# Performance work log

Hardware: AMD Instinct MI355X
Metric: run time of the kernel (lower is better)

Reference implementation:

```python
import jax, jax.numpy as jnp
import numpy as np
from jax import lax

TAU = 2.0
V_TH = 1.0
ALPHA = 4.0   # spikingjelly surrogate.Sigmoid default
BN_EPS = 1e-5
HEADS = 8


def lif(x):
    """Multi-step LIF neuron (tau=2, v_reset=0, hard reset, detach_reset).
    x: [T, ...] -> spikes [T, ...]. Forward is Heaviside; sigmoid surrogate
    is wired in via straight-through for the bwd variant."""
    def step(v, xt):
        v = v + (xt - v) / TAU                      # charge
        sg = jax.nn.sigmoid(ALPHA * (v - V_TH))     # surrogate
        hard = (v >= V_TH).astype(x.dtype)
        spike = sg + lax.stop_gradient(hard - sg)   # fwd: hard, bwd: sigmoid'
        v = v * (1.0 - lax.stop_gradient(spike))    # detached hard reset to 0
        return v, spike
    _, s = lax.scan(step, jnp.zeros_like(x[0]), x)
    return s


def conv1x1_bn(x, w, g, b, m, var, bias=None):
    # x: [N, C, H, W]; 1x1 conv == channel matmul, then eval-mode BN
    y = jnp.einsum('nchw,dc->ndhw', x, w)
    if bias is not None:
        y = y + bias[None, :, None, None]
    scale = g / jnp.sqrt(var + BN_EPS)
    shift = b - m * scale
    return y * scale[None, :, None, None] + shift[None, :, None, None]


def to_heads(x, T, B, C, H, W):
    # [T,B,C,H,W] -> [T,B,heads,N,hd]
    N = H * W
    hd = C // HEADS
    x = x.reshape(T, B, C, N).transpose(0, 1, 3, 2)          # [T,B,N,C]
    return x.reshape(T, B, N, HEADS, hd).transpose(0, 1, 3, 2, 4)


def _forward(x, q_w, q_bn_g, q_bn_b, q_bn_m, q_bn_v,
             k_w, k_bn_g, k_bn_b, k_bn_m, k_bn_v,
             v_w, v_bn_g, v_bn_b, v_bn_m, v_bn_v,
             out_w, out_b, out_bn_g, out_bn_b, out_bn_m, out_bn_v):
    T, B, C, H, W = x.shape
    N = H * W
    identity = x

    xs = lif(x)                                  # shortcut_lif
    x_qkv = xs.reshape(T * B, C, H, W)

    q = lif(conv1x1_bn(x_qkv, q_w, q_bn_g, q_bn_b, q_bn_m, q_bn_v).reshape(T, B, C, H, W))
    k = lif(conv1x1_bn(x_qkv, k_w, k_bn_g, k_bn_b, k_bn_m, k_bn_v).reshape(T, B, C, H, W))
    v = lif(conv1x1_bn(x_qkv, v_w, v_bn_g, v_bn_b, v_bn_m, v_bn_v).reshape(T, B, C, H, W))

    qh = to_heads(q, T, B, C, H, W)              # [T,B,h,N,hd]
    kh = to_heads(k, T, B, C, H, W)
    vh = to_heads(v, T, B, C, H, W)

    kv = jnp.sum(kh * vh, axis=-2, keepdims=True)   # [T,B,h,1,hd]
    kv = lif(kv)                                    # talking_heads_proj_lif
    y = qh * kv                                     # [T,B,h,N,hd]

    # [T,B,h,N,hd] -> transpose(3,4) -> [T,B,h,hd,N] -> [T,B,C,H,W]
    y = y.transpose(0, 1, 2, 4, 3).reshape(T, B, C, H, W)
    y = conv1x1_bn(y.reshape(T * B, C, H, W), out_w, out_bn_g, out_bn_b,
                   out_bn_m, out_bn_v, bias=out_b).reshape(T, B, C, H, W)
    return y + identity, vh


def setup_inputs() -> dict:
    key = jax.random.key(0)
    ks = jax.random.split(key, 6)
    T, B, C, H, W = 4, 32, 512, 14, 14
    inp = {
        'x': jax.random.normal(ks[0], (T, B, C, H, W), dtype=jnp.float32),
        'q_w': jax.random.normal(ks[1], (C, C), dtype=jnp.float32) * 0.05,
        'k_w': jax.random.normal(ks[2], (C, C), dtype=jnp.float32) * 0.05,
        'v_w': jax.random.normal(ks[3], (C, C), dtype=jnp.float32) * 0.05,
        'out_w': jax.random.normal(ks[4], (C, C), dtype=jnp.float32) * 0.05,
        'out_b': jnp.zeros((C,), dtype=jnp.float32),
    }
    for p in ('q', 'k', 'v', 'out'):
        inp[f'{p}_bn_g'] = jnp.ones((C,), dtype=jnp.float32)
        inp[f'{p}_bn_b'] = jnp.zeros((C,), dtype=jnp.float32)
        inp[f'{p}_bn_m'] = jnp.zeros((C,), dtype=jnp.float32)
        inp[f'{p}_bn_v'] = jnp.ones((C,), dtype=jnp.float32)
    return inp


def reference(x, q_w, q_bn_g, q_bn_b, q_bn_m, q_bn_v,
              k_w, k_bn_g, k_bn_b, k_bn_m, k_bn_v,
              v_w, v_bn_g, v_bn_b, v_bn_m, v_bn_v,
              out_w, out_b, out_bn_g, out_bn_b, out_bn_m, out_bn_v):
    return _forward(x, q_w, q_bn_g, q_bn_b, q_bn_m, q_bn_v,
                    k_w, k_bn_g, k_bn_b, k_bn_m, k_bn_v,
                    v_w, v_bn_g, v_bn_b, v_bn_m, v_bn_v,
                    out_w, out_b, out_bn_g, out_bn_b, out_bn_m, out_bn_v)
```

## Files before the change

kernel.cpp:

```cpp
#include <hip/hip_runtime.h>
#include <math.h>

#define T_   4
#define B_   32
#define C_   512
#define N_   196
#define TB_  128
#define M_   25088
#define BNP_ 6272
#define OUT1_ 12845056

typedef unsigned short ushort_t;
typedef __attribute__((ext_vector_type(8)))  __bf16 bf16x8;
typedef __attribute__((ext_vector_type(16))) float  f32x16;

__device__ __forceinline__ ushort_t f2bf(float f) {
    unsigned int u = __float_as_uint(f);
    u = u + 0x7FFFu + ((u >> 16) & 1u);
    return (ushort_t)(u >> 16);
}
__device__ __forceinline__ float bf2f(ushort_t h) {
    return __uint_as_float(((unsigned int)h) << 16);
}

#define GL2LDS(gp, lp) \
    __builtin_amdgcn_global_load_lds((const __attribute__((address_space(1))) void*)(gp), \
                                     (__attribute__((address_space(3))) void*)(lp), 16, 0, 0)

__global__ __launch_bounds__(256)
void prep_lifx_kernel(
    const float* __restrict__ qw, const float* __restrict__ kw,
    const float* __restrict__ vw, const float* __restrict__ ow,
    const float* __restrict__ qg, const float* __restrict__ qb, const float* __restrict__ qm, const float* __restrict__ qv,
    const float* __restrict__ kg, const float* __restrict__ kb, const float* __restrict__ km, const float* __restrict__ kvr,
    const float* __restrict__ vg, const float* __restrict__ vb, const float* __restrict__ vm, const float* __restrict__ vv,
    const float* __restrict__ og, const float* __restrict__ ob, const float* __restrict__ om, const float* __restrict__ ov,
    const float* __restrict__ obias,
    ushort_t* __restrict__ wsplit, ushort_t* __restrict__ osplit,
    float* __restrict__ scale_qkv, float* __restrict__ shift_qkv,
    float* __restrict__ scale_o,   float* __restrict__ shift_o,
    float* __restrict__ kvpart,
    const float* __restrict__ x, ushort_t* __restrict__ xs)
{
    __shared__ ushort_t tile[64 * 66];
    const int bid = blockIdx.x;
    const int tid = threadIdx.x;

    if (bid < 3072) {
        int i = bid * 256 + tid;
        int d = i >> 9, c = i & 511;
        const float* src = (d < 512) ? qw : (d < 1024) ? kw : vw;
        float wv = src[(d & 511) * 512 + c];
        ushort_t h = f2bf(wv);
        float r1 = wv - bf2f(h);
        ushort_t mm = f2bf(r1);
        wsplit[((size_t)d * 2 + 0) * 512 + c] = h;
        wsplit[((size_t)d * 2 + 1) * 512 + c] = mm;
        if (d < 512)
            osplit[(size_t)d * 512 + c] = f2bf(ow[d * 512 + c]);

        if (i < 3 * C_) {
            int p = i >> 9, dl = i & 511;
            const float* g = (p == 0) ? qg : (p == 1) ? kg : vg;
            const float* b = (p == 0) ? qb : (p == 1) ? kb : vb;
            const float* m = (p == 0) ? qm : (p == 1) ? km : vm;
            const float* r = (p == 0) ? qv : (p == 1) ? kvr : vv;
            float sc = g[dl] / sqrtf(r[dl] + 1e-5f);
            scale_qkv[i] = sc;
            shift_qkv[i] = b[dl] - m[dl] * sc;
        }
        if (i < C_) {
            float sc = og[i] / sqrtf(ov[i] + 1e-5f);
            scale_o[i] = sc;
            shift_o[i] = ob[i] - om[i] * sc + obias[i] * sc;
        }
        if (i < TB_ * C_) kvpart[i] = 0.f;
        return;
    }

    const int l = bid - 3072;
    const int n0 = (l & 3) * 64;
    const int c0 = ((l >> 2) & 7) * 64;
    const int b  = l >> 5;
    const int j = tid & 63, w = tid >> 6;
    const bool nok = (n0 + j) < N_;
    float v[16];
#pragma unroll
    for (int r = 0; r < 16; ++r) v[r] = 0.f;
    for (int t = 0; t < T_; ++t) {
        const float* xb = x + ((size_t)((t * B_ + b) * C_ + c0)) * N_ + n0 + j;
#pragma unroll
        for (int r = 0; r < 16; ++r) {
            int i = w * 16 + r;
            float xv = nok ? xb[(size_t)i * N_] : 0.f;
            v[r] = v[r] + (xv - v[r]) * 0.5f;
            bool s = (v[r] >= 1.0f);
            tile[j * 66 + i] = s ? 0x3F80 : 0;
            if (s) v[r] = 0.f;
        }
        __syncthreads();
#pragma unroll
        for (int p = 0; p < 2; ++p) {
            int w2 = tid + p * 256;
            int jj = w2 >> 3, ck = w2 & 7;
            if (n0 + jj < N_) {
                const unsigned int* src = reinterpret_cast<const unsigned int*>(&tile[jj * 66 + ck * 8]);
                uint4 dv; dv.x = src[0]; dv.y = src[1]; dv.z = src[2]; dv.w = src[3];
                size_t mp = (size_t)(b * N_ + n0 + jj) * 4 + t;
                *reinterpret_cast<uint4*>(&xs[mp * 512 + c0 + ck * 8]) = dv;
            }
        }
        __syncthreads();
    }
}

__global__ __launch_bounds__(512, 4)
void qkv_gemm_lif(const ushort_t* __restrict__ W, const ushort_t* __restrict__ X,
                  const float* __restrict__ scale, const float* __restrict__ shift,
                  float* __restrict__ out2,
                  unsigned* __restrict__ qbit, unsigned* __restrict__ kbit,
                  unsigned* __restrict__ vbit)
{
    const int id = blockIdx.x;
    const int xw = id & 7, local = id >> 3;
    const int ml = local / 12, d_t = local - ml * 12;
    const int m_t = ml * 8 + xw;
    if (m_t >= 98) return;
    const int m0 = m_t * 256;
    const int d0 = d_t * 128;

    __shared__ ushort_t Xs[2][16 * 512];
    __shared__ ushort_t Ws[2][16 * 512];
    const int tid = threadIdx.x, wid = tid >> 6, lane = tid & 63;
    const int mw = (wid & 3) * 64, dw = (wid >> 2) * 64;
    const int row32 = lane & 31, khalf = lane >> 5;

    f32x16 acc[2][2] = {};

    auto STAGE = [&](int buf, int k0) {
        {   int q = wid, mb = q >> 1, ks = q & 1;
            const ushort_t* g = X + (size_t)(m0 + mb * 32 + row32) * 512 + k0 + ks * 16 + khalf * 8;
            GL2LDS(g, &Xs[buf][q * 512]);
        }
        {   int q = wid + 8, mb = q >> 1, ks = q & 1;
            const ushort_t* g = X + (size_t)(m0 + mb * 32 + row32) * 512 + k0 + ks * 16 + khalf * 8;
            GL2LDS(g, &Xs[buf][q * 512]);
        }
        {   int q = wid, s = q >> 3, rem = q & 7, db = rem >> 1, ks = rem & 1;
            const ushort_t* g = W + ((size_t)(d0 + db * 32 + row32) * 2 + s) * 512 + k0 + ks * 16 + khalf * 8;
            GL2LDS(g, &Ws[buf][q * 512]);
        }
        {   int q = wid + 8, s = q >> 3, rem = q & 7, db = rem >> 1, ks = rem & 1;
            const ushort_t* g = W + ((size_t)(d0 + db * 32 + row32) * 2 + s) * 512 + k0 + ks * 16 + khalf * 8;
            GL2LDS(g, &Ws[buf][q * 512]);
        }
    };

    STAGE(0, 0);
    __syncthreads();
    int cur = 0;

    for (int it = 0; it < 16; ++it) {
        if (it < 15) STAGE(cur ^ 1, (it + 1) * 32);

        __builtin_amdgcn_s_setprio(1);
#pragma unroll
        for (int ks = 0; ks < 2; ++ks) {
            bf16x8 xfr[2];
#pragma unroll
            for (int i = 0; i < 2; ++i)
                xfr[i] = *reinterpret_cast<const bf16x8*>(
                    &Xs[cur][(((mw >> 5) + i) * 2 + ks) * 512 + lane * 8]);
#pragma unroll
            for (int s = 0; s < 2; ++s)
#pragma unroll
                for (int j = 0; j < 2; ++j) {
                    bf16x8 wfr = *reinterpret_cast<const bf16x8*>(
                        &Ws[cur][(s * 8 + ((dw >> 5) + j) * 2 + ks) * 512 + lane * 8]);
#pragma unroll
                    for (int i = 0; i < 2; ++i)
                        acc[i][j] = __builtin_amdgcn_mfma_f32_32x32x16_bf16(xfr[i], wfr, acc[i][j], 0, 0, 0);
                }
        }
        __builtin_amdgcn_s_setprio(0);
        __syncthreads();
        cur ^= 1;
    }

    const int p = d0 >> 9;
    const bool isV = (p == 2);
    unsigned* __restrict__ bitp = (p == 0) ? qbit : (p == 1) ? kbit : vbit;
#pragma unroll
    for (int j = 0; j < 2; ++j) {
        int d = d0 + dw + j * 32 + row32;
        float sc = scale[d], sh = shift[d];
        int dl = d & 511;
        int h = dl >> 6, hd = dl & 63;
        int cw = ((d0 & 511) + dw + j * 32) >> 5;
#pragma unroll
        for (int i = 0; i < 2; ++i) {
            int bnb = (m0 + mw + i * 32) >> 2;
            f32x16 a = acc[i][j];
#pragma unroll
            for (int g = 0; g < 4; ++g) {
                int bn = bnb + 2 * g + khalf;
                float p0 = fmaf(a[4 * g + 0], sc, sh);
                float p1 = fmaf(a[4 * g + 1], sc, sh);
                float p2 = fmaf(a[4 * g + 2], sc, sh);
                float p3 = fmaf(a[4 * g + 3], sc, sh);
                float v = p0 * 0.5f;
                bool s0 = (v >= 1.f); if (s0) v = 0.f;
                v = v + (p1 - v) * 0.5f;
                bool s1 = (v >= 1.f); if (s1) v = 0.f;
                v = v + (p2 - v) * 0.5f;
                bool s2 = (v >= 1.f); if (s2) v = 0.f;
                v = v + (p3 - v) * 0.5f;
                bool s3 = (v >= 1.f);

                const int bn_e = bnb + 2 * g;
                bool sarr[4] = {s0, s1, s2, s3};
#pragma unroll
                for (int t = 0; t < 4; ++t) {
                    unsigned long long bm = __ballot(sarr[t]);
                    if (lane == 0)
                        bitp[((size_t)t * BNP_ + bn_e) * 16 + cw] = (unsigned)bm;
                    else if (lane == 32)
                        bitp[((size_t)t * BNP_ + bn_e + 1) * 16 + cw] = (unsigned)(bm >> 32);
                }
                if (isV) {
                    int b = bn / N_, n = bn - b * N_;
                    float* o = out2 + (((size_t)b * 8 + h) * N_ + n) * 64 + hd;
                    o[0]                       = s0 ? 1.f : 0.f;
                    o[(size_t)1 * (OUT1_ / 4)] = s1 ? 1.f : 0.f;
                    o[(size_t)2 * (OUT1_ / 4)] = s2 ? 1.f : 0.f;
                    o[(size_t)3 * (OUT1_ / 4)] = s3 ? 1.f : 0.f;
                }
            }
        }
    }
}

__global__ __launch_bounds__(256)
void kv_count_kernel(const unsigned* __restrict__ kbit, const unsigned* __restrict__ vbit,
                     float* __restrict__ kvpart)
{
    __shared__ unsigned andw[98 * 16];
    const int tid = threadIdx.x;
    const int tb = blockIdx.x >> 1, half = blockIdx.x & 1;
    const int t = tb >> 5, b = tb & 31;
    const size_t wbase = ((size_t)t * BNP_ + (size_t)b * N_ + half * 98) * 16;

    const uint4* k4 = reinterpret_cast<const uint4*>(kbit + wbase);
    const uint4* v4 = reinterpret_cast<const uint4*>(vbit + wbase);
    for (int w = tid; w < 392; w += 256) {
        uint4 kq = k4[w], vq = v4[w];
        uint4 aq; aq.x = kq.x & vq.x; aq.y = kq.y & vq.y;
        aq.z = kq.z & vq.z; aq.w = kq.w & vq.w;
        *reinterpret_cast<uint4*>(&andw[w * 4]) = aq;
    }
    __syncthreads();

#pragma unroll
    for (int u = 0; u < 2; ++u) {
        int c = tid + u * 256;
        int cw = c >> 5, bit = c & 31;
        int cnt = 0;
        for (int r = 0; r < 98; ++r)
            cnt += (int)((andw[r * 16 + cw] >> bit) & 1u);
        if (cnt) atomicAdd(&kvpart[tb * 512 + c], (float)cnt);
    }
}

__global__ void kv_lif_kernel(const float* __restrict__ kvpart, ushort_t* __restrict__ kvs)
{
    int i = blockIdx.x * 256 + threadIdx.x;
    if (i >= B_ * C_) return;
    int b = i >> 9, c = i & 511;
    float v = 0.f;
#pragma unroll
    for (int t = 0; t < T_; ++t) {
        float y = kvpart[((t * B_ + b) << 9) + c];
        v = v + (y - v) * 0.5f;
        bool s = (v >= 1.f);
        kvs[((t * B_ + b) << 9) + c] = s ? 0x3F80 : 0;
        if (s) v = 0.f;
    }
}

__global__ __launch_bounds__(256)
void out_gemm(const ushort_t* __restrict__ A, const unsigned* __restrict__ qbit,
              const ushort_t* __restrict__ kvs,
              const float* __restrict__ scale, const float* __restrict__ shift,
              const float* __restrict__ xid, float* __restrict__ out)
{
    const int id = blockIdx.x;
    const int xw = id & 7, local = id >> 3;
    const int m_t = (local >> 2) * 8 + xw, d_t = local & 3;
    if (m_t >= 196) return;
    const int m0 = m_t * 128, d0 = d_t * 128;

    __shared__ ushort_t As[2][8 * 512];
    __shared__ ushort_t Bs[2][8 * 512];
    const int tid = threadIdx.x, wid = tid >> 6, lane = tid & 63;
    const int dw = (wid >> 1) * 64, mw = (wid & 1) * 64;
    const int row32 = lane & 31, khalf = lane >> 5;

    int sm[2], stb[2], sq[2], sL[2];
#pragma unroll
    for (int u = 0; u < 2; ++u) {
        int s = tid + u * 256;
        sq[u] = s >> 6; sL[u] = s & 63;
        sm[u] = m0 + (sq[u] >> 1) * 32 + (sL[u] & 31);
        stb[u] = sm[u] / N_;
    }

    f32x16 acc[2][2] = {};

    auto EXPAND = [&](int u, int kk) -> uint4 {
        unsigned qw_ = qbit[(size_t)sm[u] * 16 + (kk >> 5)];
        unsigned q8 = (qw_ >> (kk & 31)) & 0xFFu;
        uint4 kv = *reinterpret_cast<const uint4*>(&kvs[(size_t)stb[u] * 512 + kk]);
        uint4 o;
        o.x = kv.x & (((q8 & 1u)   ? 0x0000FFFFu : 0u) | ((q8 & 2u)   ? 0xFFFF0000u : 0u));
        o.y = kv.y & (((q8 & 4u)   ? 0x0000FFFFu : 0u) | ((q8 & 8u)   ? 0xFFFF0000u : 0u));
        o.z = kv.z & (((q8 & 16u)  ? 0x0000FFFFu : 0u) | ((q8 & 32u)  ? 0xFFFF0000u : 0u));
        o.w = kv.w & (((q8 & 64u)  ? 0x0000FFFFu : 0u) | ((q8 & 128u) ? 0xFFFF0000u : 0u));
        return o;
    };

    {
        uint4 o[2];
#pragma unroll
        for (int u = 0; u < 2; ++u) {
            int kk = (sq[u] & 1) * 16 + (sL[u] >> 5) * 8;
            o[u] = EXPAND(u, kk);
        }
        for (int q = wid; q < 8; q += 4) {
            int db = q >> 1, ks2 = q & 1;
            const ushort_t* g = A + (size_t)(d0 + db * 32 + row32) * 512 + ks2 * 16 + khalf * 8;
            GL2LDS(g, &As[0][q * 512]);
        }
#pragma unroll
        for (int u = 0; u < 2; ++u)
            *reinterpret_cast<uint4*>(&Bs[0][sq[u] * 512 + sL[u] * 8]) = o[u];
    }
    __syncthreads();

    int buf = 0;
    for (int it = 0; it < 16; ++it) {
        uint4 nb[2];
        if (it < 15) {
            int k0n = (it + 1) * 32;
#pragma unroll
            for (int u = 0; u < 2; ++u) {
                int kk = k0n + (sq[u] & 1) * 16 + (sL[u] >> 5) * 8;
                nb[u] = EXPAND(u, kk);
            }
            for (int q = wid; q < 8; q += 4) {
                int db = q >> 1, ks2 = q & 1;
                const ushort_t* g = A + (size_t)(d0 + db * 32 + row32) * 512 + k0n + ks2 * 16 + khalf * 8;
                GL2LDS(g, &As[buf ^ 1][q * 512]);
            }
        }

        __builtin_amdgcn_s_setprio(1);
#pragma unroll
        for (int ks = 0; ks < 2; ++ks) {
            bf16x8 afr[2];
#pragma unroll
            for (int i = 0; i < 2; ++i)
                afr[i] = *reinterpret_cast<const bf16x8*>(
                    &As[buf][(((dw >> 5) + i) * 2 + ks) * 512 + lane * 8]);
#pragma unroll
            for (int j = 0; j < 2; ++j) {
                bf16x8 bfr = *reinterpret_cast<const bf16x8*>(
                    &Bs[buf][(((mw >> 5) + j) * 2 + ks) * 512 + lane * 8]);
#pragma unroll
                for (int i = 0; i < 2; ++i)
                    acc[i][j] = __builtin_amdgcn_mfma_f32_32x32x16_bf16(afr[i], bfr, acc[i][j], 0, 0, 0);
            }
        }
        __builtin_amdgcn_s_setprio(0);

        if (it < 15) {
#pragma unroll
            for (int u = 0; u < 2; ++u)
                *reinterpret_cast<uint4*>(&Bs[buf ^ 1][sq[u] * 512 + sL[u] * 8]) = nb[u];
        }
        __syncthreads();
        buf ^= 1;
    }

#pragma unroll
    for (int j = 0; j < 2; ++j) {
        int m = m0 + mw + j * 32 + row32;
        int tb = m / N_;
        int n  = m - tb * N_;
        size_t mbase = (size_t)tb * (C_ * N_) + n;
#pragma unroll
        for (int i = 0; i < 2; ++i) {
            int dbase = d0 + dw + i * 32 + 4 * khalf;
            f32x16 a = acc[i][j];
#pragma unroll
            for (int g = 0; g < 4; ++g) {
#pragma unroll
                for (int t = 0; t < 4; ++t) {
                    int d = dbase + t + 8 * g;
                    float val = fmaf(a[4 * g + t], scale[d], shift[d]);
                    size_t ad = mbase + (size_t)d * N_;
                    out[ad] = val + xid[ad];
                }
            }
        }
    }
}

extern "C" void kernel_launch(void* const* d_in, const int* in_sizes, int n_in,
                              void* d_out, int out_size, void* d_ws, size_t ws_size,
                              hipStream_t stream)
{
    const float* x    = (const float*)d_in[0];
    const float* q_w  = (const float*)d_in[1];
    const float* k_w  = (const float*)d_in[2];
    const float* v_w  = (const float*)d_in[3];
    const float* o_w  = (const float*)d_in[4];
    const float* o_b  = (const float*)d_in[5];
    const float* qg = (const float*)d_in[6],  *qb = (const float*)d_in[7],
               *qm = (const float*)d_in[8],  *qv = (const float*)d_in[9];
    const float* kg = (const float*)d_in[10], *kb = (const float*)d_in[11],
               *km = (const float*)d_in[12], *kv = (const float*)d_in[13];
    const float* vg = (const float*)d_in[14], *vb = (const float*)d_in[15],
               *vm = (const float*)d_in[16], *vv = (const float*)d_in[17];
    const float* og = (const float*)d_in[18], *ob = (const float*)d_in[19],
               *om = (const float*)d_in[20], *ov = (const float*)d_in[21];

    float* out1  = (float*)d_out;
    float* out2f = out1 + OUT1_;

    ushort_t* spk    = (ushort_t*)d_ws;
    ushort_t* xs     = spk + (size_t)3 * M_ * 512;
    ushort_t* wsplit = xs + (size_t)M_ * 512;
    ushort_t* osplit = wsplit + (size_t)1536 * 2 * 512;
    float*    kvpart = (float*)(osplit + (size_t)512 * 512);
    ushort_t* kvs    = (ushort_t*)(kvpart + TB_ * C_);
    float*    scq    = (float*)(kvs + TB_ * C_);
    float*    shq    = scq + 3 * C_;
    float*    sco    = shq + 3 * C_;
    float*    sho    = sco + C_;

    unsigned* qbit = (unsigned*)spk;
    unsigned* kbit = (unsigned*)(spk + (size_t)M_ * 512);
    unsigned* vbit = (unsigned*)(spk + (size_t)2 * M_ * 512);

    prep_lifx_kernel<<<4096, 256, 0, stream>>>(
        q_w, k_w, v_w, o_w,
        qg, qb, qm, qv, kg, kb, km, kv, vg, vb, vm, vv, og, ob, om, ov, o_b,
        wsplit, osplit, scq, shq, sco, sho, kvpart, x, xs);

    qkv_gemm_lif<<<1200, 512, 0, stream>>>(wsplit, xs, scq, shq, out2f, qbit, kbit, vbit);

    kv_count_kernel<<<256, 256, 0, stream>>>(kbit, vbit, kvpart);

    kv_lif_kernel<<<64, 256, 0, stream>>>(kvpart, kvs);

    out_gemm<<<800, 256, 0, stream>>>(osplit, qbit, kvs, sco, sho, x, out1);
}
```

Before: 413.7 us.

## Precompute q∧kv bf16 operand in separate kernel, stage both GEMM operands via direct LDS loads

The per-tile bit expansion of q spikes masked by kv spikes is moved out of the output GEMM into a new expand kernel. That kernel writes a dense bf16 matrix of size M×512 into the reused xs buffer, and kv spikes are packed as bitmasks using ballot. The output GEMM then streams both A and B operands with global-to-LDS loads, which removes register staging and the ALU expansion from its main loop. The cost is an extra kernel launch plus about 25 MB of extra global write and read traffic.

```diff
diff --git a/kernel.cpp b/kernel.cpp
--- a/kernel.cpp
+++ b/kernel.cpp
@@ -271,25 +271,53 @@
     }
 }
 
-__global__ void kv_lif_kernel(const float* __restrict__ kvpart, ushort_t* __restrict__ kvs)
+__global__ __launch_bounds__(256)
+void kv_lif_kernel(const float* __restrict__ kvpart, unsigned* __restrict__ kvbits)
 {
     int i = blockIdx.x * 256 + threadIdx.x;
-    if (i >= B_ * C_) return;
     int b = i >> 9, c = i & 511;
+    int lane = threadIdx.x & 63;
     float v = 0.f;
 #pragma unroll
     for (int t = 0; t < T_; ++t) {
         float y = kvpart[((t * B_ + b) << 9) + c];
         v = v + (y - v) * 0.5f;
         bool s = (v >= 1.f);
-        kvs[((t * B_ + b) << 9) + c] = s ? 0x3F80 : 0;
+        unsigned long long bm = __ballot(s);
+        if (lane == 0)
+            kvbits[(t * 32 + b) * 16 + (c >> 5)] = (unsigned)bm;
+        else if (lane == 32)
+            kvbits[(t * 32 + b) * 16 + (c >> 5)] = (unsigned)(bm >> 32);
         if (s) v = 0.f;
     }
 }
 
 __global__ __launch_bounds__(256)
-void out_gemm(const ushort_t* __restrict__ A, const unsigned* __restrict__ qbit,
-              const ushort_t* __restrict__ kvs,
+void expand_kernel(const unsigned* __restrict__ qbit, const unsigned* __restrict__ kvbits,
+                   ushort_t* __restrict__ muly)
+{
+    int w = blockIdx.x * 256 + threadIdx.x;
+    int m = w >> 4, cw = w & 15;
+    int tb = m / N_;
+    unsigned bits = qbit[w] & kvbits[tb * 16 + cw];
+    uint4 o[4];
+#pragma unroll
+    for (int g = 0; g < 4; ++g) {
+        unsigned e[4];
+#pragma unroll
+        for (int i2 = 0; i2 < 4; ++i2) {
+            int p = g * 8 + i2 * 2;
+            unsigned t2 = ((bits >> p) & 1u) | (((bits >> (p + 1)) & 1u) << 16);
+            e[i2] = t2 * 0x3F80u;
+        }
+        o[g].x = e[0]; o[g].y = e[1]; o[g].z = e[2]; o[g].w = e[3];
+    }
+    uint4* dst = reinterpret_cast<uint4*>(muly + (size_t)m * 512 + cw * 32);
+    dst[0] = o[0]; dst[1] = o[1]; dst[2] = o[2]; dst[3] = o[3];
+}
+
+__global__ __launch_bounds__(256)
+void out_gemm(const ushort_t* __restrict__ A, const ushort_t* __restrict__ muly,
               const float* __restrict__ scale, const float* __restrict__ shift,
               const float* __restrict__ xid, float* __restrict__ out)
 {
@@ -305,63 +333,33 @@
     const int dw = (wid >> 1) * 64, mw = (wid & 1) * 64;
     const int row32 = lane & 31, khalf = lane >> 5;
 
-    int sm[2], stb[2], sq[2], sL[2];
-#pragma unroll
-    for (int u = 0; u < 2; ++u) {
-        int s = tid + u * 256;
-        sq[u] = s >> 6; sL[u] = s & 63;
-        sm[u] = m0 + (sq[u] >> 1) * 32 + (sL[u] & 31);
-        stb[u] = sm[u] / N_;
-    }
-
     f32x16 acc[2][2] = {};
 
-    auto EXPAND = [&](int u, int kk) -> uint4 {
-        unsigned qw_ = qbit[(size_t)sm[u] * 16 + (kk >> 5)];
-        unsigned q8 = (qw_ >> (kk & 31)) & 0xFFu;
-        uint4 kv = *reinterpret_cast<const uint4*>(&kvs[(size_t)stb[u] * 512 + kk]);
-        uint4 o;
-        o.x = kv.x & (((q8 & 1u)   ? 0x0000FFFFu : 0u) | ((q8 & 2u)   ? 0xFFFF0000u : 0u));
-        o.y = kv.y & (((q8 & 4u)   ? 0x0000FFFFu : 0u) | ((q8 & 8u)   ? 0xFFFF0000u : 0u));
-        o.z = kv.z & (((q8 & 16u)  ? 0x0000FFFFu : 0u) | ((q8 & 32u)  ? 0xFFFF0000u : 0u));
-        o.w = kv.w & (((q8 & 64u)  ? 0x0000FFFFu : 0u) | ((q8 & 128u) ? 0xFFFF0000u : 0u));
-        return o;
+    auto STAGE = [&](int buf, int k0) {
+        {   int q = wid, db = q >> 1, ks2 = q & 1;
+            const ushort_t* g = A + (size_t)(d0 + db * 32 + row32) * 512 + k0 + ks2 * 16 + khalf * 8;
+            GL2LDS(g, &As[buf][q * 512]);
+        }
+        {   int q = wid + 4, db = q >> 1, ks2 = q & 1;
+            const ushort_t* g = A + (size_t)(d0 + db * 32 + row32) * 512 + k0 + ks2 * 16 + khalf * 8;
+            GL2LDS(g, &As[buf][q * 512]);
+        }
+        {   int q = wid, mb = q >> 1, ks2 = q & 1;
+            const ushort_t* g = muly + (size_t)(m0 + mb * 32 + row32) * 512 + k0 + ks2 * 16 + khalf * 8;
+            GL2LDS(g, &Bs[buf][q * 512]);
+        }
+        {   int q = wid + 4, mb = q >> 1, ks2 = q & 1;
+            const ushort_t* g = muly + (size_t)(m0 + mb * 32 + row32) * 512 + k0 + ks2 * 16 + khalf * 8;
+            GL2LDS(g, &Bs[buf][q * 512]);
+        }
     };
 
-    {
-        uint4 o[2];
-#pragma unroll
-        for (int u = 0; u < 2; ++u) {
-            int kk = (sq[u] & 1) * 16 + (sL[u] >> 5) * 8;
-            o[u] = EXPAND(u, kk);
-        }
-        for (int q = wid; q < 8; q += 4) {
-            int db = q >> 1, ks2 = q & 1;
-            const ushort_t* g = A + (size_t)(d0 + db * 32 + row32) * 512 + ks2 * 16 + khalf * 8;
-            GL2LDS(g, &As[0][q * 512]);
-        }
-#pragma unroll
-        for (int u = 0; u < 2; ++u)
-            *reinterpret_cast<uint4*>(&Bs[0][sq[u] * 512 + sL[u] * 8]) = o[u];
-    }
+    STAGE(0, 0);
     __syncthreads();
-
     int buf = 0;
+
     for (int it = 0; it < 16; ++it) {
-        uint4 nb[2];
-        if (it < 15) {
-            int k0n = (it + 1) * 32;
-#pragma unroll
-            for (int u = 0; u < 2; ++u) {
-                int kk = k0n + (sq[u] & 1) * 16 + (sL[u] >> 5) * 8;
-                nb[u] = EXPAND(u, kk);
-            }
-            for (int q = wid; q < 8; q += 4) {
-                int db = q >> 1, ks2 = q & 1;
-                const ushort_t* g = A + (size_t)(d0 + db * 32 + row32) * 512 + k0n + ks2 * 16 + khalf * 8;
-                GL2LDS(g, &As[buf ^ 1][q * 512]);
-            }
-        }
+        if (it < 15) STAGE(buf ^ 1, (it + 1) * 32);
 
         __builtin_amdgcn_s_setprio(1);
 #pragma unroll
@@ -381,12 +379,6 @@
             }
         }
         __builtin_amdgcn_s_setprio(0);
-
-        if (it < 15) {
-#pragma unroll
-            for (int u = 0; u < 2; ++u)
-                *reinterpret_cast<uint4*>(&Bs[buf ^ 1][sq[u] * 512 + sL[u] * 8]) = nb[u];
-        }
         __syncthreads();
         buf ^= 1;
     }
@@ -448,9 +440,11 @@
     float*    sco    = shq + 3 * C_;
     float*    sho    = sco + C_;
 
-    unsigned* qbit = (unsigned*)spk;
-    unsigned* kbit = (unsigned*)(spk + (size_t)M_ * 512);
-    unsigned* vbit = (unsigned*)(spk + (size_t)2 * M_ * 512);
+    unsigned* qbit   = (unsigned*)spk;
+    unsigned* kbit   = (unsigned*)(spk + (size_t)M_ * 512);
+    unsigned* vbit   = (unsigned*)(spk + (size_t)2 * M_ * 512);
+    unsigned* kvbits = (unsigned*)kvs;
+    ushort_t* muly   = xs;
 
     prep_lifx_kernel<<<4096, 256, 0, stream>>>(
         q_w, k_w, v_w, o_w,
@@ -461,7 +455,9 @@
 
     kv_count_kernel<<<256, 256, 0, stream>>>(kbit, vbit, kvpart);
 
-    kv_lif_kernel<<<64, 256, 0, stream>>>(kvpart, kvs);
-
-    out_gemm<<<800, 256, 0, stream>>>(osplit, qbit, kvs, sco, sho, x, out1);
-}
+    kv_lif_kernel<<<64, 256, 0, stream>>>(kvpart, kvbits);
+
+    expand_kernel<<<1568, 256, 0, stream>>>(qbit, kvbits, muly);
+
+    out_gemm<<<800, 256, 0, stream>>>(osplit, muly, sco, sho, x, out1);
+}
```

After: 391.4 us (median of 3 runs). -5.4%, faster.
